# Optimization experiments

Measured on AMD Instinct MI355X. Metric: run time of the kernel, lower is better.

The kernel has to match this reference:

```python
import jax, jax.numpy as jnp
import numpy as np

TEMPERATURE = 0.1


def setup_inputs() -> dict:
    key = jax.random.key(0)
    k1, k2 = jax.random.split(key)
    N, D = 8192, 128
    features = jax.random.normal(k1, (N, D), dtype=jnp.float32)
    labels = jax.random.randint(k2, (N,), 0, 1000, dtype=jnp.int64)
    return {"features": features, "labels": labels}


def reference(features, labels):
    N = features.shape[0]
    # L2-normalize rows
    feats = features / jnp.linalg.norm(features, axis=1, keepdims=True)
    # positive-pair mask from labels [N, N]
    labels = labels.reshape(-1, 1)
    mask = (labels == labels.T).astype(feats.dtype)
    # similarity matrix scaled by temperature
    sim = jnp.matmul(feats, feats.T) / TEMPERATURE
    # exclude self-comparisons (diagonal)
    logits_mask = 1.0 - jnp.eye(N, dtype=feats.dtype)
    mask = mask * logits_mask
    exp_logits = jnp.exp(sim) * logits_mask
    log_prob = sim - jnp.log(exp_logits.sum(axis=1, keepdims=True) + 1e-9)
    mask_sum = mask.sum(axis=1)
    mask_sum = jnp.where(mask_sum == 0, jnp.ones_like(mask_sum), mask_sum)
    mean_log_prob_pos = (mask * log_prob).sum(axis=1) / mask_sum
    return -mean_log_prob_pos.mean()
```

## Files before the change

### kernel.cpp

```cpp
#include <hip/hip_runtime.h>
#include <hip/hip_bf16.h>
#include <math.h>


constexpr int N = 8192;
constexpr int D = 128;

typedef __attribute__((ext_vector_type(8))) short short8;
typedef __attribute__((ext_vector_type(4))) float f32x4;

__device__ __forceinline__ float fast_exp2(float x) {
#if __has_builtin(__builtin_amdgcn_exp2f)
    return __builtin_amdgcn_exp2f(x);
#else
    return __expf(x * 0.69314718056f);
#endif
}

__device__ __forceinline__ void gload_lds16(const void* g, void* s) {
    __builtin_amdgcn_global_load_lds(
        (const __attribute__((address_space(1))) unsigned int*)g,
        (__attribute__((address_space(3))) unsigned int*)s, 16, 0, 0);
}

__device__ __forceinline__ void stage_tile(const unsigned short* __restrict__ src,
                                           unsigned short* dst, int row0,
                                           int w, int lr, int lq) {
#pragma unroll
    for (int it = 0; it < 8; ++it) {
        int rbase = w * 32 + it * 4;
        int r = rbase + lr;
        int q = lq ^ (r & 7);
        gload_lds16(src + ((size_t)(row0 + r) * D + q * 8), dst + rbase * D);
    }
}

__global__ void prep_kernel(const float* __restrict__ F,
                            unsigned short* __restrict__ Fb,
                            float* __restrict__ rowExp,
                            float* __restrict__ rowPos) {
    int row = blockIdx.x * 4 + (threadIdx.x >> 6);
    int l = threadIdx.x & 63;
    float2 v = ((const float2*)(F + (size_t)row * D))[l];
    float ss = v.x * v.x + v.y * v.y;
#pragma unroll
    for (int off = 32; off > 0; off >>= 1) ss += __shfl_xor(ss, off);
    float sc = sqrtf(14.4269504089f / ss);
    __hip_bfloat16 hx = __float2bfloat16(v.x * sc);
    __hip_bfloat16 hy = __float2bfloat16(v.y * sc);
    ushort2 u;
    u.x = *(unsigned short*)&hx;
    u.y = *(unsigned short*)&hy;
    ((ushort2*)(Fb + (size_t)row * D))[l] = u;
    if (l == 0) {
        rowExp[row] = 0.0f;
        rowPos[row] = 0.0f;
    }
}

__global__ __launch_bounds__(256, 2) void sim_kernel(
    const unsigned short* __restrict__ Fb, const int* __restrict__ labels,
    float* __restrict__ rowExp, float* __restrict__ rowPos) {
    __shared__ unsigned short At[128 * D];
    __shared__ unsigned short Bt[128 * D];

    const int ti = blockIdx.x >> 4;
    const int g  = blockIdx.x & 15;
    const int tjs = g * 4;
    const int i0 = ti * 128;

    const int t = threadIdx.x, w = t >> 6, l = t & 63;
    const int lr = l >> 4, lq = l & 15;
    const int c = l & 15, quad = l >> 4;
    const int wy = w >> 1, wx = w & 1;

    stage_tile(Fb, At, i0, w, lr, lq);
    stage_tile(Fb, Bt, tjs * 128, w, lr, lq);

    int li[4][4];
#pragma unroll
    for (int m = 0; m < 4; ++m)
#pragma unroll
        for (int r = 0; r < 4; ++r)
            li[m][r] = labels[i0 + wy * 64 + m * 16 + quad * 4 + r];

    float RE[4][4] = {}, RP[4][4] = {};

    for (int tj = tjs; tj < tjs + 4; ++tj) {
        __syncthreads();
        const int j0 = tj * 128;
        int lj[4];
#pragma unroll
        for (int n = 0; n < 4; ++n) lj[n] = labels[j0 + wx * 64 + n * 16 + c];

        f32x4 acc[4][4] = {};
#pragma unroll
        for (int kk = 0; kk < 4; ++kk) {
            short8 af[4], bf[4];
            int sl = (kk * 4 + quad) ^ (c & 7);
#pragma unroll
            for (int m = 0; m < 4; ++m) {
                af[m] = *(const short8*)&At[(wy * 64 + m * 16 + c) * D + sl * 8];
                bf[m] = *(const short8*)&Bt[(wx * 64 + m * 16 + c) * D + sl * 8];
            }
#pragma unroll
            for (int m = 0; m < 4; ++m)
#pragma unroll
                for (int n = 0; n < 4; ++n)
                    acc[m][n] = __builtin_amdgcn_mfma_f32_16x16x32_bf16(
                        af[m], bf[n], acc[m][n], 0, 0, 0);
        }
        __syncthreads();
        if (tj < tjs + 3) stage_tile(Fb, Bt, (tj + 1) * 128, w, lr, lq);

        const bool diag = (tj == ti);
#pragma unroll
        for (int m = 0; m < 4; ++m) {
#pragma unroll
            for (int n = 0; n < 4; ++n) {
#pragma unroll
                for (int r = 0; r < 4; ++r) {
                    float s2 = acc[m][n][r];
                    bool self = diag && ((wy * 64 + m * 16 + quad * 4 + r) ==
                                         (wx * 64 + n * 16 + c));
                    float e = self ? 0.0f : fast_exp2(s2);
                    float p = (!self && li[m][r] == lj[n]) ? s2 : 0.0f;
                    RE[m][r] += e;
                    RP[m][r] += p;
                }
            }
        }
    }

#pragma unroll
    for (int m = 0; m < 4; ++m)
#pragma unroll
        for (int r = 0; r < 4; ++r) {
#pragma unroll
            for (int off = 1; off < 16; off <<= 1) {
                RE[m][r] += __shfl_xor(RE[m][r], off);
                RP[m][r] += __shfl_xor(RP[m][r], off);
            }
        }
    if (c == 0) {
#pragma unroll
        for (int m = 0; m < 4; ++m)
#pragma unroll
            for (int r = 0; r < 4; ++r) {
                int gi = i0 + wy * 64 + m * 16 + quad * 4 + r;
                atomicAdd(&rowExp[gi], RE[m][r]);
                atomicAdd(&rowPos[gi], RP[m][r]);
            }
    }
}

__global__ void finalize_kernel(const float* __restrict__ rowExp,
                                const float* __restrict__ rowPos,
                                const int* __restrict__ labels,
                                float* __restrict__ out) {
    __shared__ int hist[1024];
    __shared__ float ws16[16];
    int t = threadIdx.x;
    hist[t] = 0;
    __syncthreads();
    int lab[8];
#pragma unroll
    for (int k = 0; k < 8; ++k) {
        lab[k] = labels[t + 1024 * k];
        atomicAdd(&hist[lab[k]], 1);
    }
    __syncthreads();
    float a = 0.0f;
#pragma unroll
    for (int k = 0; k < 8; ++k) {
        int i = t + 1024 * k;
        int cnt = hist[lab[k]] - 1;
        if (cnt > 0)
            a += logf(rowExp[i] + 1e-9f) -
                 0.69314718056f * rowPos[i] / (float)cnt;
    }
#pragma unroll
    for (int off = 32; off > 0; off >>= 1) a += __shfl_xor(a, off);
    if ((t & 63) == 0) ws16[t >> 6] = a;
    __syncthreads();
    if (t == 0) {
        float s = 0.0f;
#pragma unroll
        for (int i = 0; i < 16; ++i) s += ws16[i];
        out[0] = s / (float)N;
    }
}

extern "C" void kernel_launch(void* const* d_in, const int* in_sizes, int n_in,
                              void* d_out, int out_size, void* d_ws, size_t ws_size,
                              hipStream_t stream) {
    const float* F      = (const float*)d_in[0];
    const int*   labels = (const int*)d_in[1];
    float* out = (float*)d_out;

    unsigned short* Fb = (unsigned short*)d_ws;
    float* rowExp = (float*)(Fb + (size_t)N * D);
    float* rowPos = rowExp + N;

    prep_kernel<<<N / 4, 256, 0, stream>>>(F, Fb, rowExp, rowPos);
    sim_kernel<<<64 * 16, 256, 0, stream>>>(Fb, labels, rowExp, rowPos);
    finalize_kernel<<<1, 1024, 0, stream>>>(rowExp, rowPos, labels, out);
}
```

Before: 106.9 us.

## Prepack features into MFMA fragment layout and load operands directly from global

The prep kernel now writes the normalized bf16 features in a fragment-packed layout, so each lane's MFMA operand is one contiguous 16-byte chunk. The sim kernel drops LDS staging and barriers. It keeps the A fragments in registers for the whole block and loads B fragments straight from global/L2 with coalesced loads. This removes LDS traffic and __syncthreads, at the cost of more registers and exposed global-load latency with no explicit prefetch.

```diff
diff --git a/kernel.cpp b/kernel.cpp
--- a/kernel.cpp
+++ b/kernel.cpp
@@ -17,26 +17,8 @@
 #endif
 }
 
-__device__ __forceinline__ void gload_lds16(const void* g, void* s) {
-    __builtin_amdgcn_global_load_lds(
-        (const __attribute__((address_space(1))) unsigned int*)g,
-        (__attribute__((address_space(3))) unsigned int*)s, 16, 0, 0);
-}
-
-__device__ __forceinline__ void stage_tile(const unsigned short* __restrict__ src,
-                                           unsigned short* dst, int row0,
-                                           int w, int lr, int lq) {
-#pragma unroll
-    for (int it = 0; it < 8; ++it) {
-        int rbase = w * 32 + it * 4;
-        int r = rbase + lr;
-        int q = lq ^ (r & 7);
-        gload_lds16(src + ((size_t)(row0 + r) * D + q * 8), dst + rbase * D);
-    }
-}
-
 __global__ void prep_kernel(const float* __restrict__ F,
-                            unsigned short* __restrict__ Fb,
+                            unsigned int* __restrict__ FbP,
                             float* __restrict__ rowExp,
                             float* __restrict__ rowPos) {
     int row = blockIdx.x * 4 + (threadIdx.x >> 6);
@@ -48,10 +30,11 @@
     float sc = sqrtf(14.4269504089f / ss);
     __hip_bfloat16 hx = __float2bfloat16(v.x * sc);
     __hip_bfloat16 hy = __float2bfloat16(v.y * sc);
-    ushort2 u;
-    u.x = *(unsigned short*)&hx;
-    u.y = *(unsigned short*)&hy;
-    ((ushort2*)(Fb + (size_t)row * D))[l] = u;
+    unsigned int ux = *(unsigned short*)&hx;
+    unsigned int uy = *(unsigned short*)&hy;
+    unsigned int idx = ((unsigned)(row >> 4) << 10) | ((unsigned)(l >> 2) << 6) |
+                       ((unsigned)(row & 15) << 2) | (unsigned)(l & 3);
+    FbP[idx] = ux | (uy << 16);
     if (l == 0) {
         rowExp[row] = 0.0f;
         rowPos[row] = 0.0f;
@@ -59,23 +42,23 @@
 }
 
 __global__ __launch_bounds__(256, 2) void sim_kernel(
-    const unsigned short* __restrict__ Fb, const int* __restrict__ labels,
+    const short8* __restrict__ P, const int* __restrict__ labels,
     float* __restrict__ rowExp, float* __restrict__ rowPos) {
-    __shared__ unsigned short At[128 * D];
-    __shared__ unsigned short Bt[128 * D];
-
     const int ti = blockIdx.x >> 4;
     const int g  = blockIdx.x & 15;
     const int tjs = g * 4;
     const int i0 = ti * 128;
 
     const int t = threadIdx.x, w = t >> 6, l = t & 63;
-    const int lr = l >> 4, lq = l & 15;
     const int c = l & 15, quad = l >> 4;
     const int wy = w >> 1, wx = w & 1;
 
-    stage_tile(Fb, At, i0, w, lr, lq);
-    stage_tile(Fb, Bt, tjs * 128, w, lr, lq);
+    short8 Af[4][4];
+#pragma unroll
+    for (int kk = 0; kk < 4; ++kk)
+#pragma unroll
+        for (int m = 0; m < 4; ++m)
+            Af[kk][m] = P[(ti * 8 + wy * 4 + m) * 256 + kk * 64 + l];
 
     int li[4][4];
 #pragma unroll
@@ -87,7 +70,6 @@
     float RE[4][4] = {}, RP[4][4] = {};
 
     for (int tj = tjs; tj < tjs + 4; ++tj) {
-        __syncthreads();
         const int j0 = tj * 128;
         int lj[4];
 #pragma unroll
@@ -96,22 +78,17 @@
         f32x4 acc[4][4] = {};
 #pragma unroll
         for (int kk = 0; kk < 4; ++kk) {
-            short8 af[4], bf[4];
-            int sl = (kk * 4 + quad) ^ (c & 7);
+            short8 bf[4];
 #pragma unroll
-            for (int m = 0; m < 4; ++m) {
-                af[m] = *(const short8*)&At[(wy * 64 + m * 16 + c) * D + sl * 8];
-                bf[m] = *(const short8*)&Bt[(wx * 64 + m * 16 + c) * D + sl * 8];
-            }
+            for (int n = 0; n < 4; ++n)
+                bf[n] = P[(tj * 8 + wx * 4 + n) * 256 + kk * 64 + l];
 #pragma unroll
             for (int m = 0; m < 4; ++m)
 #pragma unroll
                 for (int n = 0; n < 4; ++n)
                     acc[m][n] = __builtin_amdgcn_mfma_f32_16x16x32_bf16(
-                        af[m], bf[n], acc[m][n], 0, 0, 0);
+                        Af[kk][m], bf[n], acc[m][n], 0, 0, 0);
         }
-        __syncthreads();
-        if (tj < tjs + 3) stage_tile(Fb, Bt, (tj + 1) * 128, w, lr, lq);
 
         const bool diag = (tj == ti);
 #pragma unroll
@@ -198,11 +175,12 @@
     const int*   labels = (const int*)d_in[1];
     float* out = (float*)d_out;
 
-    unsigned short* Fb = (unsigned short*)d_ws;
-    float* rowExp = (float*)(Fb + (size_t)N * D);
+    unsigned int* FbP = (unsigned int*)d_ws;
+    float* rowExp = (float*)((unsigned short*)d_ws + (size_t)N * D);
     float* rowPos = rowExp + N;
 
-    prep_kernel<<<N / 4, 256, 0, stream>>>(F, Fb, rowExp, rowPos);
-    sim_kernel<<<64 * 16, 256, 0, stream>>>(Fb, labels, rowExp, rowPos);
+    prep_kernel<<<N / 4, 256, 0, stream>>>(F, FbP, rowExp, rowPos);
+    sim_kernel<<<64 * 16, 256, 0, stream>>>((const short8*)FbP, labels, rowExp,
+                                            rowPos);
     finalize_kernel<<<1, 1024, 0, stream>>>(rowExp, rowPos, labels, out);
 }
```

Measured after the change: 106.9 us. Within noise of the previous version (-0.1%).
